# Kernel tuning notes

Measured on AMD Instinct MI355X. Metric: run time of the kernel, lower is better.

The kernel has to match this reference:

```python
import jax, jax.numpy as jnp
import numpy as np

B, T, H, L = 64, 256, 512, 2

def setup_inputs() -> dict:
    key = jax.random.key(0)
    ks = jax.random.split(key, 5)
    s = 0.05  # keep gate pre-activations in a sane range
    return {
        "x": jax.random.normal(ks[0], (B, T, H), jnp.float32),
        "Wi": jax.random.normal(ks[1], (L, H, 4 * H), jnp.float32) * s,
        "Wh": jax.random.normal(ks[2], (L, H, 4 * H), jnp.float32) * s,
        "bi": jax.random.normal(ks[3], (L, 4 * H), jnp.float32) * s,
        "bh": jax.random.normal(ks[4], (L, 4 * H), jnp.float32) * s,
    }

def _lstm(x, Wi, Wh, bi, bh):
    b, t, _ = x.shape
    L_, H_ = Wi.shape[0], Wi.shape[2] // 4
    h0 = jnp.zeros((L_, b, H_), x.dtype)
    c0 = jnp.zeros((L_, b, H_), x.dtype)

    def step(carry, x_t):
        h, c = carry
        hs, cs = [], []
        inp = x_t  # [B, H]
        for l in range(L_):
            gates = inp @ Wi[l] + bi[l] + h[l] @ Wh[l] + bh[l]  # [B, 4H]
            i, f, g, o = jnp.split(gates, 4, axis=-1)
            i, f, o = jax.nn.sigmoid(i), jax.nn.sigmoid(f), jax.nn.sigmoid(o)
            g = jnp.tanh(g)
            new_c = f * c[l] + i * g
            new_h = o * jnp.tanh(new_c)
            hs.append(new_h)
            cs.append(new_c)
            inp = new_h
        return (jnp.stack(hs), jnp.stack(cs)), inp

    (hT, cT), outs = jax.lax.scan(step, (h0, c0), jnp.swapaxes(x, 0, 1))
    return jnp.swapaxes(outs, 0, 1), (hT, cT)  # [B,T,H], ([L,B,H],[L,B,H])

def reference(x, Wi, Wh, bi, bh):
    return _lstm(x, Wi, Wh, bi, bh)
```

## Files before the change

### kernel.cpp

```cpp
#include <hip/hip_runtime.h>

typedef __attribute__((ext_vector_type(8))) short short8;
typedef __attribute__((ext_vector_type(4))) float f32x4;
typedef __attribute__((ext_vector_type(4))) int   i32x4;
typedef __attribute__((ext_vector_type(4))) float fvec4;
typedef __attribute__((ext_vector_type(4))) unsigned short u16x4;

#define B_ 64
#define T_ 256
#define H_ 512
#define NG 2048
#define BTH (64*256*512)
#define BH (64*512)

__device__ __forceinline__ float bf2f(unsigned short u) {
    return __builtin_bit_cast(float, ((unsigned)u) << 16);
}
__device__ __forceinline__ unsigned short f2bf(float f) {
    unsigned u = __builtin_bit_cast(unsigned, f);
    u += 0x7fffu + ((u >> 16) & 1u);
    return (unsigned short)(u >> 16);
}
__device__ __forceinline__ float sigm(float x) { return 1.f / (1.f + __expf(-x)); }
__device__ __forceinline__ float tanh_f(float x) {
    x = fminf(15.f, fmaxf(-15.f, x));
    float e = __expf(-2.f * x);
    return (1.f - e) / (1.f + e);
}

__device__ __forceinline__ void store_coh(unsigned* p, unsigned v) {
    __hip_atomic_store(p, v, __ATOMIC_RELAXED, __HIP_MEMORY_SCOPE_AGENT);
}

__global__ void transpose_cvt(const float* __restrict__ Wi, const float* __restrict__ Wh,
                              unsigned short* __restrict__ Wt) {
    __shared__ float tile[64][65];
    int z = blockIdx.z;
    const float* src = (z < 2 ? Wi : Wh) + (size_t)(z & 1) * H_ * NG;
    unsigned short* dst = Wt + (size_t)z * NG * H_;
    int k0 = blockIdx.x * 64, n0 = blockIdx.y * 64;
    int tx = threadIdx.x & 63, ty = threadIdx.x >> 6;
#pragma unroll
    for (int p = 0; p < 16; ++p) {
        int r = (p << 2) + ty;
        tile[r][tx] = src[(size_t)(k0 + r) * NG + n0 + tx];
    }
    __syncthreads();
#pragma unroll
    for (int p = 0; p < 16; ++p) {
        int r = (p << 2) + ty;
        dst[(size_t)(n0 + r) * H_ + k0 + tx] = f2bf(tile[tx][r]);
    }
}

__global__ void cvt_bf16(const float* __restrict__ x, unsigned short* __restrict__ xb) {
    size_t i = ((size_t)blockIdx.x * 256 + threadIdx.x) * 4;
    fvec4 v = *(const fvec4*)&x[i];
    u16x4 o;
    o[0] = f2bf(v[0]); o[1] = f2bf(v[1]); o[2] = f2bf(v[2]); o[3] = f2bf(v[3]);
    *(u16x4*)&xb[i] = o;
}

__global__ __launch_bounds__(256) void gemm_bt(
    const unsigned short* __restrict__ A, const unsigned short* __restrict__ Bt,
    const float* __restrict__ bias1, const float* __restrict__ bias2,
    unsigned short* __restrict__ C) {
    const int tid = threadIdx.x;
    const int wave = tid >> 6, lane = tid & 63;
    const int quad = lane >> 4, l15 = lane & 15;
    const int row0 = blockIdx.x * 64 + wave * 16;
    const int col0 = blockIdx.y * 64;
    f32x4 acc[4] = {};
    const unsigned short* ap = A + (size_t)(row0 + l15) * H_ + (quad << 3);
    const unsigned short* bp = Bt + (size_t)(col0 + l15) * H_ + (quad << 3);
#pragma unroll
    for (int kk = 0; kk < H_; kk += 32) {
        short8 a = *(const short8*)(ap + kk);
#pragma unroll
        for (int c4 = 0; c4 < 4; ++c4) {
            short8 b = *(const short8*)(bp + (size_t)(c4 << 4) * H_ + kk);
            acc[c4] = __builtin_amdgcn_mfma_f32_16x16x32_bf16(a, b, acc[c4], 0, 0, 0);
        }
    }
#pragma unroll
    for (int c4 = 0; c4 < 4; ++c4) {
        int col = col0 + (c4 << 4) + l15;
        float bs = bias1[col] + bias2[col];
#pragma unroll
        for (int r = 0; r < 4; ++r) {
            int row = row0 + (quad << 2) + r;
            int t = row & 255, b = row >> 8;
            C[((size_t)t * B_ + b) * NG + col] = f2bf(acc[c4][r] + bs);
        }
    }
}

__device__ __forceinline__ void flag_publish(unsigned* flags, int myslot, unsigned target) {
    __syncthreads();
    if (threadIdx.x == 0) store_coh(flags + myslot, target);
}
__device__ __forceinline__ void flag_wait(const unsigned* flags, unsigned target) {
    int spins = 0;
    for (;;) {
        unsigned v = __hip_atomic_load(flags + (threadIdx.x & 31), __ATOMIC_RELAXED,
                                       __HIP_MEMORY_SCOPE_AGENT);
        if (__all((int)(v >= target))) break;
        __builtin_amdgcn_s_sleep(1);
        if (++spins > 400000) break;
    }
    asm volatile("" ::: "memory");
}

__global__ __launch_bounds__(256, 1) void lstm_fused(
    const unsigned short* __restrict__ Gi,
    const unsigned short* __restrict__ Wt,
    unsigned* __restrict__ h0h,
    unsigned* __restrict__ h1h,
    const float* __restrict__ bi, const float* __restrict__ bh,
    float* __restrict__ out,
    float* __restrict__ hT, float* __restrict__ cT,
    unsigned* __restrict__ flags) {
    __shared__ unsigned short wi_lds[64 * 512];
    const size_t NK = (size_t)NG * H_;
    const int tid = threadIdx.x;
    const int wave = tid >> 6, lane = tid & 63;
    const int quad = lane >> 4, l15 = lane & 15;
    const int m0 = wave << 4;
    unsigned* flag0 = flags;
    unsigned* flag1 = flags + 32;

    if (blockIdx.x < 32) {
        const int slot = (int)blockIdx.x;
        const int j0 = slot << 4;
        const unsigned short* Wht = Wt + 2 * NK;
        short8 bw[64];
#pragma unroll
        for (int kb = 0; kb < 16; ++kb)
#pragma unroll
            for (int g = 0; g < 4; ++g)
                bw[kb * 4 + g] =
                    *(const short8*)&Wht[(size_t)((g << 9) + j0 + l15) * H_ + (kb << 5) + (quad << 3)];
#pragma unroll
        for (int i = 0; i < 64; ++i) asm volatile("" : "+v"(bw[i]));

        if (!(l15 & 1)) {
#pragma unroll
            for (int r = 0; r < 4; ++r) {
                int b = m0 + (quad << 2) + r;
                store_coh(&h0h[(b << 8) + ((j0 + l15) >> 1)], 0u);
            }
        }
        float cc[4] = {0.f, 0.f, 0.f, 0.f};

        flag_publish(flag0, slot, 1u);
        float gv[4][4];
#pragma unroll
        for (int r = 0; r < 4; ++r) {
            int b = m0 + (quad << 2) + r;
#pragma unroll
            for (int g = 0; g < 4; ++g)
                gv[g][r] = bf2f(Gi[(size_t)b * NG + (g << 9) + j0 + l15]);
        }
        flag_wait(flag0, 1u);

        for (int t = 0; t < T_; ++t) {
            const unsigned* ap = h0h + ((size_t)t << 14) + ((m0 + l15) << 8) + (quad << 2);
            short8 ha[16];
#pragma unroll
            for (int kb = 0; kb < 16; ++kb) ha[kb] = *(const short8*)(ap + (kb << 4));

            f32x4 acc0 = {}, acc1 = {}, acc2 = {}, acc3 = {};
#pragma unroll
            for (int kb = 0; kb < 16; ++kb) {
                acc0 = __builtin_amdgcn_mfma_f32_16x16x32_bf16(ha[kb], bw[kb * 4 + 0], acc0, 0, 0, 0);
                acc1 = __builtin_amdgcn_mfma_f32_16x16x32_bf16(ha[kb], bw[kb * 4 + 1], acc1, 0, 0, 0);
                acc2 = __builtin_amdgcn_mfma_f32_16x16x32_bf16(ha[kb], bw[kb * 4 + 2], acc2, 0, 0, 0);
                acc3 = __builtin_amdgcn_mfma_f32_16x16x32_bf16(ha[kb], bw[kb * 4 + 3], acc3, 0, 0, 0);
            }

            float hvv[4];
#pragma unroll
            for (int r = 0; r < 4; ++r) {
                int b = m0 + (quad << 2) + r;
                int jj = j0 + l15;
                float iv = sigm(acc0[r] + gv[0][r]);
                float fv = sigm(acc1[r] + gv[1][r]);
                float gg = tanh_f(acc2[r] + gv[2][r]);
                float ov = sigm(acc3[r] + gv[3][r]);
                float cn = fv * cc[r] + iv * gg;
                cc[r] = cn;
                float hv = ov * tanh_f(cn);
                hvv[r] = hv;
                unsigned short hb16 = f2bf(hv);
                unsigned packed = (unsigned)hb16 |
                                  (((unsigned)(unsigned short)__shfl_xor((int)hb16, 1)) << 16);
                if (!(l15 & 1))
                    store_coh(&h0h[((size_t)(t + 1) << 14) + (b << 8) + (jj >> 1)], packed);
            }

            flag_publish(flag0, slot, (unsigned)(t + 2));
            int tn = (t + 1) & (T_ - 1);
            float gn[4][4];
#pragma unroll
            for (int r = 0; r < 4; ++r) {
                int b = m0 + (quad << 2) + r;
#pragma unroll
                for (int g = 0; g < 4; ++g)
                    gn[g][r] = bf2f(Gi[((size_t)tn * B_ + b) * NG + (g << 9) + j0 + l15]);
            }
            if (t == T_ - 1) {
#pragma unroll
                for (int r = 0; r < 4; ++r) {
                    int b = m0 + (quad << 2) + r;
                    int jj = j0 + l15;
                    hT[((size_t)b << 9) + jj] = hvv[r];
                    cT[((size_t)b << 9) + jj] = cc[r];
                }
            }
            flag_wait(flag0, (unsigned)(t + 2));
#pragma unroll
            for (int r = 0; r < 4; ++r)
#pragma unroll
                for (int g = 0; g < 4; ++g) gv[g][r] = gn[g][r];
        }
    } else {
        const int slot = (int)blockIdx.x - 32;
        const int j0 = slot << 4;
        const unsigned short* Wht = Wt + 3 * NK;
        short8 bw[64];
#pragma unroll
        for (int kb = 0; kb < 16; ++kb)
#pragma unroll
            for (int g = 0; g < 4; ++g)
                bw[kb * 4 + g] =
                    *(const short8*)&Wht[(size_t)((g << 9) + j0 + l15) * H_ + (kb << 5) + (quad << 3)];
#pragma unroll
        for (int i = 0; i < 64; ++i) asm volatile("" : "+v"(bw[i]));

        const unsigned short* Wit = Wt + 1 * NK;
#pragma unroll
        for (int i2 = 0; i2 < 16; ++i2) {
            int c = i2 * 256 + tid;
            int l = c & 15, q = (c >> 4) & 3, g = (c >> 6) & 3, kb = c >> 8;
            short8 v = *(const short8*)&Wit[(size_t)((g << 9) + j0 + l) * H_ + (kb << 5) + (q << 3)];
            *(short8*)((char*)wi_lds + ((size_t)c << 4)) = v;
        }
        const int wbase = (quad << 8) + (l15 << 4);

        float gb0 = bi[NG + j0 + l15]        + bh[NG + j0 + l15];
        float gb1 = bi[NG + 512 + j0 + l15]  + bh[NG + 512 + j0 + l15];
        float gb2 = bi[NG + 1024 + j0 + l15] + bh[NG + 1024 + j0 + l15];
        float gb3 = bi[NG + 1536 + j0 + l15] + bh[NG + 1536 + j0 + l15];

        if (!(l15 & 1)) {
#pragma unroll
            for (int r = 0; r < 4; ++r) {
                int b = m0 + (quad << 2) + r;
                store_coh(&h1h[(b << 8) + ((j0 + l15) >> 1)], 0u);
            }
        }
        float cc[4] = {0.f, 0.f, 0.f, 0.f};
        flag_publish(flag1, slot, 1u);
        flag_wait(flag1, 1u);

        short8 ha1[16], ha0[16];
        {
            const unsigned* ap1 = h1h + ((m0 + l15) << 8) + (quad << 2);
#pragma unroll
            for (int kb = 0; kb < 16; ++kb) ha1[kb] = *(const short8*)(ap1 + (kb << 4));
        }
        flag_wait(flag0, 2u);
        {
            const unsigned* ap0 = h0h + ((size_t)1 << 14) + ((m0 + l15) << 8) + (quad << 2);
#pragma unroll
            for (int kb = 0; kb < 16; ++kb) ha0[kb] = *(const short8*)(ap0 + (kb << 4));
        }

        for (int t = 0; t < T_; ++t) {
            f32x4 acc0 = {}, acc1 = {}, acc2 = {}, acc3 = {};
#pragma unroll
            for (int kb = 0; kb < 16; ++kb) {
                acc0 = __builtin_amdgcn_mfma_f32_16x16x32_bf16(ha1[kb], bw[kb * 4 + 0], acc0, 0, 0, 0);
                acc1 = __builtin_amdgcn_mfma_f32_16x16x32_bf16(ha1[kb], bw[kb * 4 + 1], acc1, 0, 0, 0);
                acc2 = __builtin_amdgcn_mfma_f32_16x16x32_bf16(ha1[kb], bw[kb * 4 + 2], acc2, 0, 0, 0);
                acc3 = __builtin_amdgcn_mfma_f32_16x16x32_bf16(ha1[kb], bw[kb * 4 + 3], acc3, 0, 0, 0);
            }
#pragma unroll
            for (int kb = 0; kb < 16; ++kb) {
                const char* base = (const char*)wi_lds + (kb << 12) + wbase;
                short8 w0 = *(const short8*)(base);
                short8 w1 = *(const short8*)(base + (1 << 10));
                short8 w2 = *(const short8*)(base + (2 << 10));
                short8 w3 = *(const short8*)(base + (3 << 10));
                acc0 = __builtin_amdgcn_mfma_f32_16x16x32_bf16(ha0[kb], w0, acc0, 0, 0, 0);
                acc1 = __builtin_amdgcn_mfma_f32_16x16x32_bf16(ha0[kb], w1, acc1, 0, 0, 0);
                acc2 = __builtin_amdgcn_mfma_f32_16x16x32_bf16(ha0[kb], w2, acc2, 0, 0, 0);
                acc3 = __builtin_amdgcn_mfma_f32_16x16x32_bf16(ha0[kb], w3, acc3, 0, 0, 0);
            }

            float hvv[4];
#pragma unroll
            for (int r = 0; r < 4; ++r) {
                int b = m0 + (quad << 2) + r;
                int jj = j0 + l15;
                float iv = sigm(acc0[r] + gb0);
                float fv = sigm(acc1[r] + gb1);
                float gg = tanh_f(acc2[r] + gb2);
                float ov = sigm(acc3[r] + gb3);
                float cn = fv * cc[r] + iv * gg;
                cc[r] = cn;
                float hv = ov * tanh_f(cn);
                hvv[r] = hv;
                unsigned short hb16 = f2bf(hv);
                unsigned packed = (unsigned)hb16 |
                                  (((unsigned)(unsigned short)__shfl_xor((int)hb16, 1)) << 16);
                if (!(l15 & 1))
                    store_coh(&h1h[((size_t)(t + 1) << 14) + (b << 8) + (jj >> 1)], packed);
            }

            flag_publish(flag1, slot, (unsigned)(t + 2));
#pragma unroll
            for (int r = 0; r < 4; ++r) {
                int b = m0 + (quad << 2) + r;
                int jj = j0 + l15;
                out[((size_t)((b << 8) + t)) * H_ + jj] = hvv[r];
            }
            if (t == T_ - 1) {
#pragma unroll
                for (int r = 0; r < 4; ++r) {
                    int b = m0 + (quad << 2) + r;
                    int jj = j0 + l15;
                    hT[BH + ((size_t)b << 9) + jj] = hvv[r];
                    cT[BH + ((size_t)b << 9) + jj] = cc[r];
                }
            }
            flag_wait(flag1, (unsigned)(t + 2));

            if (t < T_ - 1) {
                const unsigned* ap1 =
                    h1h + ((size_t)(t + 1) << 14) + ((m0 + l15) << 8) + (quad << 2);
#pragma unroll
                for (int kb = 0; kb < 16; ++kb) ha1[kb] = *(const short8*)(ap1 + (kb << 4));
                flag_wait(flag0, (unsigned)(t + 3));
                const unsigned* ap0 =
                    h0h + ((size_t)(t + 2) << 14) + ((m0 + l15) << 8) + (quad << 2);
#pragma unroll
                for (int kb = 0; kb < 16; ++kb) ha0[kb] = *(const short8*)(ap0 + (kb << 4));
            }
        }
    }
}

extern "C" void kernel_launch(void* const* d_in, const int* in_sizes, int n_in,
                              void* d_out, int out_size, void* d_ws, size_t ws_size,
                              hipStream_t stream) {
    const float* x  = (const float*)d_in[0];
    const float* Wi = (const float*)d_in[1];
    const float* Wh = (const float*)d_in[2];
    const float* bi = (const float*)d_in[3];
    const float* bh = (const float*)d_in[4];
    float* out = (float*)d_out;

    char* w = (char*)d_ws;
    const size_t NK = (size_t)NG * H_;
    unsigned short* Wt  = (unsigned short*)w;
    unsigned short* xb  = Wt + 4 * NK;
    unsigned short* Gi  = xb + (size_t)16384 * H_;
    unsigned* h0h       = (unsigned*)(Gi + (size_t)16384 * NG);
    unsigned* h1h       = h0h + (size_t)(T_ + 1) * 16384;
    unsigned* flags     = h1h + (size_t)(T_ + 1) * 16384;

    hipMemsetAsync(flags, 0, 256, stream);

    transpose_cvt<<<dim3(8, 32, 4), 256, 0, stream>>>(Wi, Wh, Wt);
    cvt_bf16<<<8192, 256, 0, stream>>>(x, xb);

    gemm_bt<<<dim3(256, 32), 256, 0, stream>>>(xb, Wt + 0 * NK, bi, bh, Gi);

    lstm_fused<<<64, 256, 0, stream>>>(Gi, Wt, h0h, h1h, bi, bh,
                                       out, out + BTH, out + BTH + 2 * (size_t)BH, flags);
}
```

Baseline: 2.497 ms.

## Replace block barriers with per-wave padded flags and reblock hidden-state layout

Result: faster. 2.137 ms (-14.4%).

```diff
diff --git a/kernel.cpp b/kernel.cpp
--- a/kernel.cpp
+++ b/kernel.cpp
@@ -2,7 +2,6 @@
 
 typedef __attribute__((ext_vector_type(8))) short short8;
 typedef __attribute__((ext_vector_type(4))) float f32x4;
-typedef __attribute__((ext_vector_type(4))) int   i32x4;
 typedef __attribute__((ext_vector_type(4))) float fvec4;
 typedef __attribute__((ext_vector_type(4))) unsigned short u16x4;
 
@@ -12,6 +11,7 @@
 #define NG 2048
 #define BTH (64*256*512)
 #define BH (64*512)
+#define FPAD 64
 
 __device__ __forceinline__ float bf2f(unsigned short u) {
     return __builtin_bit_cast(float, ((unsigned)u) << 16);
@@ -30,6 +30,20 @@
 
 __device__ __forceinline__ void store_coh(unsigned* p, unsigned v) {
     __hip_atomic_store(p, v, __ATOMIC_RELAXED, __HIP_MEMORY_SCOPE_AGENT);
+}
+__device__ __forceinline__ void drain_vm() {
+    asm volatile("s_waitcnt vmcnt(0)" ::: "memory");
+}
+__device__ __forceinline__ void wv_wait(const unsigned* fl, int w, unsigned target) {
+    const unsigned* p = fl + (size_t)(((threadIdx.x & 31) << 2) + w) * FPAD;
+    int spins = 0;
+    for (;;) {
+        unsigned v = __hip_atomic_load(p, __ATOMIC_RELAXED, __HIP_MEMORY_SCOPE_AGENT);
+        if (__all((int)(v >= target))) break;
+        __builtin_amdgcn_s_sleep(1);
+        if (++spins > 400000) break;
+    }
+    asm volatile("" ::: "memory");
 }
 
 __global__ void transpose_cvt(const float* __restrict__ Wi, const float* __restrict__ Wh,
@@ -86,29 +100,16 @@
     for (int c4 = 0; c4 < 4; ++c4) {
         int col = col0 + (c4 << 4) + l15;
         float bs = bias1[col] + bias2[col];
+        int g = col >> 9;
+        int blk = (col & 511) >> 4;
 #pragma unroll
         for (int r = 0; r < 4; ++r) {
             int row = row0 + (quad << 2) + r;
             int t = row & 255, b = row >> 8;
-            C[((size_t)t * B_ + b) * NG + col] = f2bf(acc[c4][r] + bs);
-        }
-    }
-}
-
-__device__ __forceinline__ void flag_publish(unsigned* flags, int myslot, unsigned target) {
-    __syncthreads();
-    if (threadIdx.x == 0) store_coh(flags + myslot, target);
-}
-__device__ __forceinline__ void flag_wait(const unsigned* flags, unsigned target) {
-    int spins = 0;
-    for (;;) {
-        unsigned v = __hip_atomic_load(flags + (threadIdx.x & 31), __ATOMIC_RELAXED,
-                                       __HIP_MEMORY_SCOPE_AGENT);
-        if (__all((int)(v >= target))) break;
-        __builtin_amdgcn_s_sleep(1);
-        if (++spins > 400000) break;
-    }
-    asm volatile("" ::: "memory");
+            C[((size_t)blk << 20) + ((size_t)t << 12) + (g << 10) + (b << 4) + l15] =
+                f2bf(acc[c4][r] + bs);
+        }
+    }
 }
 
 __global__ __launch_bounds__(256, 1) void lstm_fused(
@@ -127,7 +128,8 @@
     const int quad = lane >> 4, l15 = lane & 15;
     const int m0 = wave << 4;
     unsigned* flag0 = flags;
-    unsigned* flag1 = flags + 32;
+    unsigned* flag1 = flags + 128 * FPAD;
+    const size_t hoff = ((size_t)(quad >> 1) << 9) + ((size_t)(m0 + l15) << 3) + ((quad & 1) << 2);
 
     if (blockIdx.x < 32) {
         const int slot = (int)blockIdx.x;
@@ -144,30 +146,30 @@
         for (int i = 0; i < 64; ++i) asm volatile("" : "+v"(bw[i]));
 
         if (!(l15 & 1)) {
-#pragma unroll
-            for (int r = 0; r < 4; ++r) {
-                int b = m0 + (quad << 2) + r;
-                store_coh(&h0h[(b << 8) + ((j0 + l15) >> 1)], 0u);
-            }
+            unsigned* hz = h0h + ((size_t)(slot * 64) << 3) + (l15 >> 1);
+#pragma unroll
+            for (int r = 0; r < 4; ++r)
+                store_coh(&hz[(size_t)(m0 + (quad << 2) + r) << 3], 0u);
         }
         float cc[4] = {0.f, 0.f, 0.f, 0.f};
-
-        flag_publish(flag0, slot, 1u);
+        drain_vm();
+        store_coh(&flag0[(size_t)((slot << 2) + wave) * FPAD], 1u);
+
         float gv[4][4];
 #pragma unroll
         for (int r = 0; r < 4; ++r) {
             int b = m0 + (quad << 2) + r;
 #pragma unroll
             for (int g = 0; g < 4; ++g)
-                gv[g][r] = bf2f(Gi[(size_t)b * NG + (g << 9) + j0 + l15]);
-        }
-        flag_wait(flag0, 1u);
+                gv[g][r] = bf2f(Gi[((size_t)slot << 20) + (g << 10) + (b << 4) + l15]);
+        }
 
         for (int t = 0; t < T_; ++t) {
-            const unsigned* ap = h0h + ((size_t)t << 14) + ((m0 + l15) << 8) + (quad << 2);
+            wv_wait(flag0, wave, (unsigned)(t + 1));
+            const unsigned* ap = h0h + ((size_t)t << 14) + hoff;
             short8 ha[16];
 #pragma unroll
-            for (int kb = 0; kb < 16; ++kb) ha[kb] = *(const short8*)(ap + (kb << 4));
+            for (int kb = 0; kb < 16; ++kb) ha[kb] = *(const short8*)(ap + (kb << 10));
 
             f32x4 acc0 = {}, acc1 = {}, acc2 = {}, acc3 = {};
 #pragma unroll
@@ -178,11 +180,10 @@
                 acc3 = __builtin_amdgcn_mfma_f32_16x16x32_bf16(ha[kb], bw[kb * 4 + 3], acc3, 0, 0, 0);
             }
 
+            unsigned* hw = h0h + ((size_t)(t + 1) << 14) + ((size_t)(slot * 64) << 3) + (l15 >> 1);
             float hvv[4];
 #pragma unroll
             for (int r = 0; r < 4; ++r) {
-                int b = m0 + (quad << 2) + r;
-                int jj = j0 + l15;
                 float iv = sigm(acc0[r] + gv[0][r]);
                 float fv = sigm(acc1[r] + gv[1][r]);
                 float gg = tanh_f(acc2[r] + gv[2][r]);
@@ -195,18 +196,7 @@
                 unsigned packed = (unsigned)hb16 |
                                   (((unsigned)(unsigned short)__shfl_xor((int)hb16, 1)) << 16);
                 if (!(l15 & 1))
-                    store_coh(&h0h[((size_t)(t + 1) << 14) + (b << 8) + (jj >> 1)], packed);
-            }
-
-            flag_publish(flag0, slot, (unsigned)(t + 2));
-            int tn = (t + 1) & (T_ - 1);
-            float gn[4][4];
-#pragma unroll
-            for (int r = 0; r < 4; ++r) {
-                int b = m0 + (quad << 2) + r;
-#pragma unroll
-                for (int g = 0; g < 4; ++g)
-                    gn[g][r] = bf2f(Gi[((size_t)tn * B_ + b) * NG + (g << 9) + j0 + l15]);
+                    store_coh(&hw[(size_t)(m0 + (quad << 2) + r) << 3], packed);
             }
             if (t == T_ - 1) {
 #pragma unroll
@@ -217,11 +207,18 @@
                     cT[((size_t)b << 9) + jj] = cc[r];
                 }
             }
-            flag_wait(flag0, (unsigned)(t + 2));
-#pragma unroll
-            for (int r = 0; r < 4; ++r)
-#pragma unroll
-                for (int g = 0; g < 4; ++g) gv[g][r] = gn[g][r];
+            drain_vm();
+            store_coh(&flag0[(size_t)((slot << 2) + wave) * FPAD], (unsigned)(t + 2));
+
+            int tn = (t + 1) & (T_ - 1);
+#pragma unroll
+            for (int r = 0; r < 4; ++r) {
+                int b = m0 + (quad << 2) + r;
+#pragma unroll
+                for (int g = 0; g < 4; ++g)
+                    gv[g][r] = bf2f(Gi[((size_t)slot << 20) + ((size_t)tn << 12) +
+                                       (g << 10) + (b << 4) + l15]);
+            }
         }
     } else {
         const int slot = (int)blockIdx.x - 32;
@@ -245,6 +242,7 @@
             short8 v = *(const short8*)&Wit[(size_t)((g << 9) + j0 + l) * H_ + (kb << 5) + (q << 3)];
             *(short8*)((char*)wi_lds + ((size_t)c << 4)) = v;
         }
+        __syncthreads();
         const int wbase = (quad << 8) + (l15 << 4);
 
         float gb0 = bi[NG + j0 + l15]        + bh[NG + j0 + l15];
@@ -253,27 +251,27 @@
         float gb3 = bi[NG + 1536 + j0 + l15] + bh[NG + 1536 + j0 + l15];
 
         if (!(l15 & 1)) {
-#pragma unroll
-            for (int r = 0; r < 4; ++r) {
-                int b = m0 + (quad << 2) + r;
-                store_coh(&h1h[(b << 8) + ((j0 + l15) >> 1)], 0u);
-            }
+            unsigned* hz = h1h + ((size_t)(slot * 64) << 3) + (l15 >> 1);
+#pragma unroll
+            for (int r = 0; r < 4; ++r)
+                store_coh(&hz[(size_t)(m0 + (quad << 2) + r) << 3], 0u);
         }
         float cc[4] = {0.f, 0.f, 0.f, 0.f};
-        flag_publish(flag1, slot, 1u);
-        flag_wait(flag1, 1u);
+        drain_vm();
+        store_coh(&flag1[(size_t)((slot << 2) + wave) * FPAD], 1u);
 
         short8 ha1[16], ha0[16];
+        wv_wait(flag1, wave, 1u);
         {
-            const unsigned* ap1 = h1h + ((m0 + l15) << 8) + (quad << 2);
-#pragma unroll
-            for (int kb = 0; kb < 16; ++kb) ha1[kb] = *(const short8*)(ap1 + (kb << 4));
-        }
-        flag_wait(flag0, 2u);
+            const unsigned* ap1 = h1h + hoff;
+#pragma unroll
+            for (int kb = 0; kb < 16; ++kb) ha1[kb] = *(const short8*)(ap1 + (kb << 10));
+        }
+        wv_wait(flag0, wave, 2u);
         {
-            const unsigned* ap0 = h0h + ((size_t)1 << 14) + ((m0 + l15) << 8) + (quad << 2);
-#pragma unroll
-            for (int kb = 0; kb < 16; ++kb) ha0[kb] = *(const short8*)(ap0 + (kb << 4));
+            const unsigned* ap0 = h0h + ((size_t)1 << 14) + hoff;
+#pragma unroll
+            for (int kb = 0; kb < 16; ++kb) ha0[kb] = *(const short8*)(ap0 + (kb << 10));
         }
 
         for (int t = 0; t < T_; ++t) {
@@ -298,11 +296,10 @@
                 acc3 = __builtin_amdgcn_mfma_f32_16x16x32_bf16(ha0[kb], w3, acc3, 0, 0, 0);
             }
 
+            unsigned* hw = h1h + ((size_t)(t + 1) << 14) + ((size_t)(slot * 64) << 3) + (l15 >> 1);
             float hvv[4];
 #pragma unroll
             for (int r = 0; r < 4; ++r) {
-                int b = m0 + (quad << 2) + r;
-                int jj = j0 + l15;
                 float iv = sigm(acc0[r] + gb0);
                 float fv = sigm(acc1[r] + gb1);
                 float gg = tanh_f(acc2[r] + gb2);
@@ -315,10 +312,8 @@
                 unsigned packed = (unsigned)hb16 |
                                   (((unsigned)(unsigned short)__shfl_xor((int)hb16, 1)) << 16);
                 if (!(l15 & 1))
-                    store_coh(&h1h[((size_t)(t + 1) << 14) + (b << 8) + (jj >> 1)], packed);
-            }
-
-            flag_publish(flag1, slot, (unsigned)(t + 2));
+                    store_coh(&hw[(size_t)(m0 + (quad << 2) + r) << 3], packed);
+            }
 #pragma unroll
             for (int r = 0; r < 4; ++r) {
                 int b = m0 + (quad << 2) + r;
@@ -333,20 +328,19 @@
                     hT[BH + ((size_t)b << 9) + jj] = hvv[r];
                     cT[BH + ((size_t)b << 9) + jj] = cc[r];
                 }
-            }
-            flag_wait(flag1, (unsigned)(t + 2));
-
-            if (t < T_ - 1) {
-                const unsigned* ap1 =
-                    h1h + ((size_t)(t + 1) << 14) + ((m0 + l15) << 8) + (quad << 2);
-#pragma unroll
-                for (int kb = 0; kb < 16; ++kb) ha1[kb] = *(const short8*)(ap1 + (kb << 4));
-                flag_wait(flag0, (unsigned)(t + 3));
-                const unsigned* ap0 =
-                    h0h + ((size_t)(t + 2) << 14) + ((m0 + l15) << 8) + (quad << 2);
-#pragma unroll
-                for (int kb = 0; kb < 16; ++kb) ha0[kb] = *(const short8*)(ap0 + (kb << 4));
-            }
+                break;
+            }
+            drain_vm();
+            store_coh(&flag1[(size_t)((slot << 2) + wave) * FPAD], (unsigned)(t + 2));
+
+            wv_wait(flag0, wave, (unsigned)(t + 3));
+            const unsigned* ap0 = h0h + ((size_t)(t + 2) << 14) + hoff;
+#pragma unroll
+            for (int kb = 0; kb < 16; ++kb) ha0[kb] = *(const short8*)(ap0 + (kb << 10));
+            wv_wait(flag1, wave, (unsigned)(t + 2));
+            const unsigned* ap1 = h1h + ((size_t)(t + 1) << 14) + hoff;
+#pragma unroll
+            for (int kb = 0; kb < 16; ++kb) ha1[kb] = *(const short8*)(ap1 + (kb << 10));
         }
     }
 }
@@ -370,7 +364,7 @@
     unsigned* h1h       = h0h + (size_t)(T_ + 1) * 16384;
     unsigned* flags     = h1h + (size_t)(T_ + 1) * 16384;
 
-    hipMemsetAsync(flags, 0, 256, stream);
+    hipMemsetAsync(flags, 0, 2 * 128 * FPAD * sizeof(unsigned), stream);
 
     transpose_cvt<<<dim3(8, 32, 4), 256, 0, stream>>>(Wi, Wh, Wt);
     cvt_bf16<<<8192, 256, 0, stream>>>(x, xb);
```
